# Optimization experiments

Measured on AMD Instinct MI355X. Metric: run time of the kernel, lower is better.

Reference implementation:

```python
import jax, jax.numpy as jnp
import numpy as np
from jax import lax

EPS = 1e-5      # InstanceNorm2d default eps
SLOPE = 0.2     # LeakyReLU negative slope
K = 3           # kernel size
PAD = 1


def _conv(x, w, pad=PAD):
    # x: [B,C,H,W], w: [O,I,K,K], stride 1
    return lax.conv_general_dilated(x, w, (1, 1), [(pad, pad), (pad, pad)],
                                    dimension_numbers=('NCHW', 'OIHW', 'NCHW'))


def _instance_norm(x, gamma, beta):
    mu = jnp.mean(x, (2, 3), keepdims=True)
    var = jnp.mean((x - mu) ** 2, (2, 3), keepdims=True)
    xn = (x - mu) * lax.rsqrt(var + EPS)
    return xn * gamma[None, :, None, None] + beta[None, :, None, None]


def _lrelu(x):
    return jnp.where(x >= 0, x, SLOPE * x)


def _deform_conv(x, w_off, b_off, w_def):
    # DCNv2: offsets+mask predicted by a 3x3 conv, then modulated bilinear sampling.
    B, C, H, W = x.shape
    om = _conv(x, w_off) + b_off[None, :, None, None]       # [B, 3*K*K, H, W]
    o1, o2, m = jnp.split(om, 3, axis=1)                    # each [B, K*K, H, W]
    off = jnp.concatenate([o1, o2], axis=1)                 # [B, 2*K*K, H, W]
    dy = off[:, 0::2]                                       # [B, K*K, H, W] y-offsets
    dx = off[:, 1::2]                                       # [B, K*K, H, W] x-offsets
    mask = jax.nn.sigmoid(m)                                # [B, K*K, H, W]

    ky = jnp.repeat(jnp.arange(K), K).astype(x.dtype)       # tap row index per k
    kx = jnp.tile(jnp.arange(K), K).astype(x.dtype)         # tap col index per k
    py = dy + jnp.arange(H, dtype=x.dtype)[None, None, :, None] - PAD + ky[None, :, None, None]
    px = dx + jnp.arange(W, dtype=x.dtype)[None, None, None, :] - PAD + kx[None, :, None, None]

    y0 = jnp.floor(py); x0 = jnp.floor(px)
    ly = py - y0; lx = px - x0
    y0i = y0.astype(jnp.int32); x0i = x0.astype(jnp.int32)

    xf = x.reshape(B, C, H * W)

    def gather(iy, ix):
        valid = ((iy >= 0) & (iy < H) & (ix >= 0) & (ix < W)).astype(x.dtype)
        idx = jnp.clip(iy, 0, H - 1) * W + jnp.clip(ix, 0, W - 1)
        v = jax.vmap(lambda f, i: jnp.take(f, i, axis=-1))(xf, idx)  # [B,C,K*K,H,W]
        return v * valid[:, None]

    samp = (gather(y0i, x0i)         * ((1 - ly) * (1 - lx))[:, None]
          + gather(y0i, x0i + 1)     * ((1 - ly) * lx)[:, None]
          + gather(y0i + 1, x0i)     * (ly * (1 - lx))[:, None]
          + gather(y0i + 1, x0i + 1) * (ly * lx)[:, None])          # [B,C,K*K,H,W]

    wk = w_def.reshape(w_def.shape[0], C, K * K)            # [O,C,K*K]
    return jnp.einsum('ock,bckhw,bkhw->bohw', wk, samp, mask)


def setup_inputs() -> dict:
    key = jax.random.key(0)
    ks = jax.random.split(key, 10)
    B, C, H, W = 4, 128, 96, 96
    x = jax.random.normal(ks[0], (B, C, H, W), jnp.float32)
    g1 = 1.0 + 0.05 * jax.random.normal(ks[1], (C,), jnp.float32)
    b1 = 0.05 * jax.random.normal(ks[2], (C,), jnp.float32)
    g2 = 1.0 + 0.05 * jax.random.normal(ks[3], (C,), jnp.float32)
    b2 = 0.05 * jax.random.normal(ks[4], (C,), jnp.float32)
    w1 = jax.random.normal(ks[5], (C, C, K, K), jnp.float32) * 0.03
    bc1 = 0.01 * jax.random.normal(ks[6], (C,), jnp.float32)
    # offset/mask conv: zero-init in the original; use small random values so the
    # irregular bilinear-sampling path is actually exercised.
    w_off = jax.random.normal(ks[7], (3 * K * K, C, K, K), jnp.float32) * 0.01
    b_off = 0.01 * jax.random.normal(ks[8], (3 * K * K,), jnp.float32)
    w_def = jax.random.normal(ks[9], (C, C, K, K), jnp.float32) * 0.03  # DeformConv has bias=None
    return {"x": x, "g1": g1, "b1": b1, "g2": g2, "b2": b2,
            "w1": w1, "bc1": bc1, "w_off": w_off, "b_off": b_off, "w_def": w_def}


def reference(x, g1, b1, g2, b2, w1, bc1, w_off, b_off, w_def):
    h = _lrelu(_instance_norm(x, g1, b1))
    h = _conv(h, w1) + bc1[None, :, None, None]
    h = _lrelu(_instance_norm(h, g2, b2))
    h = _deform_conv(h, w_off, b_off, w_def)
    return h + x
```

## Files before the change

kernel.cpp:

```cpp
#include <hip/hip_runtime.h>
#include <hip/hip_fp16.h>
#include <math.h>

#define HWN 9216
#define HD 96
#define WD 96

typedef _Float16 h8v __attribute__((ext_vector_type(8)));
typedef float f16x16 __attribute__((ext_vector_type(16)));

__device__ __forceinline__ ushort f2h(float f) {
  return __half_as_ushort(__float2half(f));
}
__device__ __forceinline__ __half2 u2h(unsigned u) {
  return __builtin_bit_cast(__half2, u);
}
__device__ __forceinline__ unsigned h2u(__half2 h) {
  return __builtin_bit_cast(unsigned, h);
}
__device__ __forceinline__ h8v u4h(uint4 v) {
  return __builtin_bit_cast(h8v, v);
}
__device__ __forceinline__ f16x16 mfma32(h8v a, h8v b, f16x16 c) {
  return __builtin_amdgcn_mfma_f32_32x32x16_f16(a, b, c, 0, 0, 0);
}
__device__ __forceinline__ __half2 pkmax2(__half2 a, __half2 b) {
  unsigned r;
  asm("v_pk_max_f16 %0, %1, %2" : "=v"(r) : "v"(h2u(a)), "v"(h2u(b)));
  return u2h(r);
}
__device__ __forceinline__ __half2 lrelu2(__half2 v, __half2 c02) {
  return pkmax2(v, __hmul2(v, c02));
}

__global__ __launch_bounds__(256) void packxt_kernel(
    const float* __restrict__ w1, const float* __restrict__ wdef,
    const float* __restrict__ woff, const float* __restrict__ x,
    ushort* __restrict__ w1p, ushort* __restrict__ wdp, ushort* __restrict__ wofp,
    unsigned* __restrict__ xh, float* __restrict__ partS, float* __restrict__ partQ) {
  __shared__ float tl[128][97];
  int bid = blockIdx.x;
  int t = threadIdx.x;
  if (bid < 162) {
    int i = bid * 256 + t;
    const float* src;
    ushort* dst;
    int CT, CO_real, fi;
    if (i < 18432) { src = w1; dst = w1p; CT = 4; CO_real = 128; fi = i; }
    else if (i < 36864) { src = wdef; dst = wdp; CT = 4; CO_real = 128; fi = i - 18432; }
    else { src = woff; dst = wofp; CT = 1; CO_real = 27; fi = i - 36864; }
    int lane = fi & 63;
    int j = fi >> 6;
    int ks = j & 7; j >>= 3;
    int ct = j % CT;
    int kk = j / CT;
    int co = ct * 32 + (lane & 31);
    int c0 = ks * 16 + (lane >> 5) * 8;
    ushort fr[8];
#pragma unroll
    for (int e = 0; e < 8; ++e) {
      float v = 0.f;
      if (co < CO_real) v = src[(size_t)(co * 128 + c0 + e) * 9 + kk];
      fr[e] = f2h(v);
    }
    uint4 o4;
    o4.x = (unsigned)fr[0] | ((unsigned)fr[1] << 16);
    o4.y = (unsigned)fr[2] | ((unsigned)fr[3] << 16);
    o4.z = (unsigned)fr[4] | ((unsigned)fr[5] << 16);
    o4.w = (unsigned)fr[6] | ((unsigned)fr[7] << 16);
    *(uint4*)(dst + (size_t)fi * 8) = o4;
    return;
  }
  int xb = bid - 162;
  int b = xb / 96, y = xb % 96;
  const float* sbase = x + (size_t)b * 128 * HWN + y * WD;
  for (int i = t; i < 12288; i += 256) {
    int c = i / 96, xx = i - c * 96;
    tl[c][xx] = sbase[(size_t)c * HWN + xx];
  }
  __syncthreads();
  {
    int c = t >> 1, half = t & 1;
    float S = 0.f, Q = 0.f;
    for (int j = 0; j < 48; ++j) {
      float v = tl[c][half * 48 + j];
      S += v;
      Q += v * v;
    }
    S += __shfl_xor(S, 1, 64);
    Q += __shfl_xor(Q, 1, 64);
    if (half == 0) {
      partS[((size_t)(b * 96 + y)) * 128 + c] = S;
      partQ[((size_t)(b * 96 + y)) * 128 + c] = Q;
    }
  }
  unsigned* dbase = xh + (size_t)(b * 96 + y) * 96 * 64;
  for (int i = t; i < 6144; i += 256) {
    int xx = i >> 6, c2 = i & 63;
    unsigned lo = f2h(tl[2 * c2][xx]);
    unsigned hi = f2h(tl[2 * c2 + 1][xx]);
    dbase[xx * 64 + c2] = lo | (hi << 16);
  }
}

__global__ __launch_bounds__(64) void finalize_kernel(
    const float* __restrict__ partS, const float* __restrict__ partQ,
    const float* __restrict__ gamma, const float* __restrict__ beta,
    float* __restrict__ sa_, float* __restrict__ sb_, int ntiles) {
  int bc = blockIdx.x;
  int b = bc >> 7, c = bc & 127;
  float S = 0.f, Q = 0.f;
  for (int tl = threadIdx.x; tl < ntiles; tl += 64) {
    S += partS[((size_t)b * ntiles + tl) * 128 + c];
    Q += partQ[((size_t)b * ntiles + tl) * 128 + c];
  }
#pragma unroll
  for (int off = 32; off > 0; off >>= 1) {
    S += __shfl_down(S, off, 64);
    Q += __shfl_down(Q, off, 64);
  }
  if (threadIdx.x == 0) {
    float mu = S / (float)HWN;
    float var = Q / (float)HWN - mu * mu;
    float rs = rsqrtf(var + 1e-5f);
    float a = rs * gamma[c];
    sa_[bc] = a;
    sb_[bc] = beta[c] - mu * a;
  }
}

__global__ __launch_bounds__(512) void conv1_mfma(
    const ushort* __restrict__ inp, const float* __restrict__ sa_,
    const float* __restrict__ sb_, const ushort* __restrict__ wp,
    const float* __restrict__ bias, ushort* __restrict__ outh,
    float* __restrict__ partS, float* __restrict__ partQ) {
  __shared__ ushort halo[100 * 128];
  __shared__ __half2 sah[64], sbh[64];
  int b = blockIdx.y;
  int tile = blockIdx.x;
  int Y0 = (tile / 12) * 8, X0 = (tile % 12) * 8;
  int t = threadIdx.x;
  int lane = t & 63, w = t >> 6;
  if (t < 64) {
    sah[t] = __floats2half2_rn(sa_[b * 128 + 2 * t], sa_[b * 128 + 2 * t + 1]);
    sbh[t] = __floats2half2_rn(sb_[b * 128 + 2 * t], sb_[b * 128 + 2 * t + 1]);
  }
  __syncthreads();
  const __half2 c02 = __float2half2_rn(0.2f);
  const ushort* ib = inp + (size_t)b * HWN * 128;
  for (int i = t; i < 400; i += 512) {
    int r = i >> 2, q = i & 3;
    int gy = Y0 - 1 + r / 10, gx = X0 - 1 + r % 10;
    bool inb = ((unsigned)gy < 96u) && ((unsigned)gx < 96u);
    const uint4* gp4 = (const uint4*)(ib + (size_t)(gy * 96 + gx) * 128 + q * 32);
#pragma unroll
    for (int cc = 0; cc < 4; ++cc) {
      uint4 v = make_uint4(0, 0, 0, 0);
      if (inb) {
        uint4 g = gp4[cc];
        unsigned ar[4] = {g.x, g.y, g.z, g.w};
        int c2b = (q * 4 + cc) * 4;
#pragma unroll
        for (int j = 0; j < 4; ++j) {
          __half2 hv = __hfma2(u2h(ar[j]), sah[c2b + j], sbh[c2b + j]);
          hv = lrelu2(hv, c02);
          ar[j] = h2u(hv);
        }
        v.x = ar[0]; v.y = ar[1]; v.z = ar[2]; v.w = ar[3];
      }
      int ch = (q * 4 + cc) ^ (r & 7);
      *(uint4*)&halo[r * 128 + ch * 8] = v;
    }
  }
  __syncthreads();

  int ct = w >> 1, pt = w & 1;
  int pl = lane & 31, kh = lane >> 5;
  int p = pt * 32 + pl;
  f16x16 acc = (f16x16)(0.f);

  uint4 Acur[8], Anxt[8];
#pragma unroll
  for (int ks = 0; ks < 8; ++ks)
    Acur[ks] = *(const uint4*)(wp + (size_t)((0 * 4 + ct) * 8 + ks) * 512 + lane * 8);

  for (int kk = 0; kk < 9; ++kk) {
    if (kk < 8) {
#pragma unroll
      for (int ks = 0; ks < 8; ++ks)
        Anxt[ks] = *(const uint4*)(wp + (size_t)(((kk + 1) * 4 + ct) * 8 + ks) * 512 + lane * 8);
    }
    int ky = kk / 3, kx = kk % 3;
    int r = ((p >> 3) + ky) * 10 + (p & 7) + kx;
    __builtin_amdgcn_s_setprio(1);
#pragma unroll
    for (int ks = 0; ks < 8; ++ks) {
      int u = (ks * 2 + kh) ^ (r & 7);
      h8v bf = *(const h8v*)&halo[r * 128 + u * 8];
      acc = mfma32(u4h(Acur[ks]), bf, acc);
    }
    __builtin_amdgcn_s_setprio(0);
    if (kk < 8) {
#pragma unroll
      for (int ks = 0; ks < 8; ++ks) Acur[ks] = Anxt[ks];
    }
  }
  int gp = (Y0 + (p >> 3)) * 96 + X0 + (p & 7);
  float s[16], q[16];
#pragma unroll
  for (int g = 0; g < 4; ++g) {
    int ch0 = ct * 32 + 4 * kh + 8 * g;
    float v0 = acc[4 * g + 0] + bias[ch0 + 0];
    float v1 = acc[4 * g + 1] + bias[ch0 + 1];
    float v2 = acc[4 * g + 2] + bias[ch0 + 2];
    float v3 = acc[4 * g + 3] + bias[ch0 + 3];
    uint2 o;
    o.x = (unsigned)f2h(v0) | ((unsigned)f2h(v1) << 16);
    o.y = (unsigned)f2h(v2) | ((unsigned)f2h(v3) << 16);
    *(uint2*)&outh[((size_t)b * HWN + gp) * 128 + ch0] = o;
    s[4 * g + 0] = v0; s[4 * g + 1] = v1; s[4 * g + 2] = v2; s[4 * g + 3] = v3;
    q[4 * g + 0] = v0 * v0; q[4 * g + 1] = v1 * v1;
    q[4 * g + 2] = v2 * v2; q[4 * g + 3] = v3 * v3;
  }
#pragma unroll
  for (int r = 0; r < 16; ++r)
#pragma unroll
    for (int m = 1; m < 32; m <<= 1) {
      s[r] += __shfl_xor(s[r], m, 64);
      q[r] += __shfl_xor(q[r], m, 64);
    }
  if (pl == 0) {
    size_t base = ((size_t)b * 288 + tile * 2 + pt) * 128;
#pragma unroll
    for (int r = 0; r < 16; ++r) {
      int co = ct * 32 + 4 * kh + (r & 3) + 8 * (r >> 2);
      partS[base + co] = s[r];
      partQ[base + co] = q[r];
    }
  }
}

__device__ __forceinline__ uint4 gaffine(const ushort* hb, int pix, int cc,
                                         const __half2* sa2v, const __half2* sb2v,
                                         __half2 c02) {
  uint4 g = *(const uint4*)(hb + (size_t)pix * 128 + cc * 8);
  unsigned ar[4] = {g.x, g.y, g.z, g.w};
#pragma unroll
  for (int j = 0; j < 4; ++j) {
    __half2 hv = __hfma2(u2h(ar[j]), sa2v[j], sb2v[j]);
    hv = lrelu2(hv, c02);
    ar[j] = h2u(hv);
  }
  return make_uint4(ar[0], ar[1], ar[2], ar[3]);
}

__global__ __launch_bounds__(256) void deform_fused(
    const ushort* __restrict__ h2n, const float* __restrict__ sa_,
    const float* __restrict__ sb_, const ushort* __restrict__ wofp,
    const float* __restrict__ boff, const ushort* __restrict__ wdp,
    const float* __restrict__ x, float* __restrict__ out) {
  __shared__ __align__(16) ushort halo[96 * 128];
  __shared__ __align__(16) ushort S[32 * 128];
  __shared__ __align__(16) ushort4 idxs[9][32];
  __shared__ __align__(16) ushort4 wgtc[9][32];
  __shared__ __half2 sah[64], sbh[64];
  float* om_t = (float*)S;
  int bid = blockIdx.x;
  int swz = (bid & 7) * 144 + (bid >> 3);
  int b = swz / 288;
  int tile = swz % 288;
  int Y0 = (tile / 12) * 4, X0 = (tile % 12) * 8;
  int t = threadIdx.x;
  int lane = t & 63, w = t >> 6;
  const ushort* hb = h2n + (size_t)b * HWN * 128;
  if (t < 64) {
    sah[t] = __floats2half2_rn(sa_[b * 128 + 2 * t], sa_[b * 128 + 2 * t + 1]);
    sbh[t] = __floats2half2_rn(sb_[b * 128 + 2 * t], sb_[b * 128 + 2 * t + 1]);
  }
  __syncthreads();
  const __half2 c02 = __float2half2_rn(0.2f);

  for (int i = t; i < 1536; i += 256) {
    int pix = i >> 4, u = i & 15;
    int gy = Y0 - 2 + pix / 12, gx = X0 - 2 + pix % 12;
    uint4 v = make_uint4(0, 0, 0, 0);
    if (((unsigned)gy < 96u) && ((unsigned)gx < 96u)) {
      uint4 g = *(const uint4*)(hb + (size_t)(gy * 96 + gx) * 128 + u * 8);
      unsigned ar[4] = {g.x, g.y, g.z, g.w};
#pragma unroll
      for (int j = 0; j < 4; ++j) {
        __half2 hv = __hfma2(u2h(ar[j]), sah[u * 4 + j], sbh[u * 4 + j]);
        hv = lrelu2(hv, c02);
        ar[j] = h2u(hv);
      }
      v.x = ar[0]; v.y = ar[1]; v.z = ar[2]; v.w = ar[3];
    }
    *(uint4*)&halo[pix * 128 + ((u ^ (pix & 15)) * 8)] = v;
  }
  __syncthreads();

  if (w == 0) {
    int pl = lane & 31, kh = lane >> 5;
    int p = pl;
    f16x16 accm = (f16x16)(0.f);
    uint4 Ac[8], An[8];
#pragma unroll
    for (int ks = 0; ks < 8; ++ks)
      Ac[ks] = *(const uint4*)(wofp + (size_t)(0 * 8 + ks) * 512 + lane * 8);
    for (int kk = 0; kk < 9; ++kk) {
      if (kk < 8) {
#pragma unroll
        for (int ks = 0; ks < 8; ++ks)
          An[ks] = *(const uint4*)(wofp + (size_t)((kk + 1) * 8 + ks) * 512 + lane * 8);
      }
      int ky = kk / 3, kx = kk % 3;
      int hp = (1 + (p >> 3) + ky) * 12 + 1 + (p & 7) + kx;
#pragma unroll
      for (int ks = 0; ks < 8; ++ks) {
        int u = (ks * 2 + kh) ^ (hp & 15);
        h8v bf = *(const h8v*)&halo[hp * 128 + u * 8];
        accm = mfma32(u4h(Ac[ks]), bf, accm);
      }
      if (kk < 8) {
#pragma unroll
        for (int ks = 0; ks < 8; ++ks) Ac[ks] = An[ks];
      }
    }
#pragma unroll
    for (int reg = 0; reg < 16; ++reg) {
      int co = 4 * kh + (reg & 3) + 8 * (reg >> 2);
      if (co < 27) om_t[co * 32 + p] = accm[reg] + boff[co];
    }
  }
  __syncthreads();

  for (int i = t; i < 288; i += 256) {
    int k = i >> 5, p = i & 31;
    int yy = Y0 + (p >> 3), xx = X0 + (p & 7);
    float dy = om_t[(2 * k) * 32 + p];
    float dx = om_t[(2 * k + 1) * 32 + p];
    float mv = om_t[(18 + k) * 32 + p];
    float mask = 1.0f / (1.0f + expf(-mv));
    float py = dy + (float)(yy - 1 + (k / 3));
    float px = dx + (float)(xx - 1 + (k % 3));
    float fy = floorf(py), fx = floorf(px);
    float lyf = py - fy, lxf = px - fx;
    int y0 = (int)fy, x0 = (int)fx;
    int y1 = y0 + 1, x1 = x0 + 1;
    bool vy0 = (y0 >= 0) && (y0 < HD);
    bool vy1 = (y1 >= 0) && (y1 < HD);
    bool vx0 = (x0 >= 0) && (x0 < WD);
    bool vx1 = (x1 >= 0) && (x1 < WD);
    int y0c = min(max(y0, 0), HD - 1), y1c = min(max(y1, 0), HD - 1);
    int x0c = min(max(x0, 0), WD - 1), x1c = min(max(x1, 0), WD - 1);
    float w0 = (1.f - lyf) * (1.f - lxf) * ((vy0 && vx0) ? mask : 0.f);
    float w1v = (1.f - lyf) * lxf * ((vy0 && vx1) ? mask : 0.f);
    float w2 = lyf * (1.f - lxf) * ((vy1 && vx0) ? mask : 0.f);
    float w3 = lyf * lxf * ((vy1 && vx1) ? mask : 0.f);
    bool inh = (y0c >= Y0 - 2) && (y1c <= Y0 + 5) && (x0c >= X0 - 2) && (x1c <= X0 + 9);
    ushort4 sidx;
    if (inh) {
      int sy0 = y0c - (Y0 - 2), sy1 = y1c - (Y0 - 2);
      int sx0 = x0c - (X0 - 2), sx1 = x1c - (X0 - 2);
      sidx.x = (ushort)(sy0 * 12 + sx0);
      sidx.y = (ushort)(sy0 * 12 + sx1);
      sidx.z = (ushort)(sy1 * 12 + sx0);
      sidx.w = (ushort)(sy1 * 12 + sx1);
    } else {
      sidx.x = (ushort)((y0c * WD + x0c) | 0x8000);
      sidx.y = (ushort)(y0c * WD + x1c);
      sidx.z = (ushort)(y1c * WD + x0c);
      sidx.w = (ushort)(y1c * WD + x1c);
    }
    idxs[k][p] = sidx;
    ushort4 wc;
    wc.x = f2h(w0); wc.y = f2h(w1v); wc.z = f2h(w2); wc.w = f2h(w3);
    wgtc[k][p] = wc;
  }
  __syncthreads();

  int cc = t & 15;
  int pp = t >> 4;
  int ct = w;
  int pl = lane & 31, kh = lane >> 5;
  int pg = pl;
  f16x16 acc = (f16x16)(0.f);
  __half2 sa2v[4], sb2v[4];
#pragma unroll
  for (int j = 0; j < 4; ++j) { sa2v[j] = sah[cc * 4 + j]; sb2v[j] = sbh[cc * 4 + j]; }

  uint4 AW[8];
  for (int k = 0; k < 9; ++k) {
    const ushort* wk = wdp + (size_t)k * 16384;
#pragma unroll
    for (int ks = 0; ks < 8; ++ks)
      AW[ks] = *(const uint4*)(wk + (size_t)(ct * 8 + ks) * 512 + lane * 8);
#pragma unroll
    for (int i2 = 0; i2 < 2; ++i2) {
      int p = pp + 16 * i2;
      ushort4 sidx = idxs[k][p];
      ushort4 wc = wgtc[k][p];
      uint4 C0, C1, C2, C3;
      if (sidx.x & 0x8000u) {
        C0 = gaffine(hb, sidx.x & 0x7fff, cc, sa2v, sb2v, c02);
        C1 = gaffine(hb, sidx.y, cc, sa2v, sb2v, c02);
        C2 = gaffine(hb, sidx.z, cc, sa2v, sb2v, c02);
        C3 = gaffine(hb, sidx.w, cc, sa2v, sb2v, c02);
      } else {
        C0 = *(const uint4*)&halo[sidx.x * 128 + ((cc ^ (sidx.x & 15)) * 8)];
        C1 = *(const uint4*)&halo[sidx.y * 128 + ((cc ^ (sidx.y & 15)) * 8)];
        C2 = *(const uint4*)&halo[sidx.z * 128 + ((cc ^ (sidx.z & 15)) * 8)];
        C3 = *(const uint4*)&halo[sidx.w * 128 + ((cc ^ (sidx.w & 15)) * 8)];
      }
      __half2 a0 = u2h((unsigned)wc.x * 0x10001u);
      __half2 a1 = u2h((unsigned)wc.y * 0x10001u);
      __half2 a2 = u2h((unsigned)wc.z * 0x10001u);
      __half2 a3 = u2h((unsigned)wc.w * 0x10001u);
      __half2 s0 = __hmul2(u2h(C0.x), a0);
      __half2 s1 = __hmul2(u2h(C0.y), a0);
      __half2 s2 = __hmul2(u2h(C0.z), a0);
      __half2 s3 = __hmul2(u2h(C0.w), a0);
      s0 = __hfma2(u2h(C1.x), a1, s0); s1 = __hfma2(u2h(C1.y), a1, s1);
      s2 = __hfma2(u2h(C1.z), a1, s2); s3 = __hfma2(u2h(C1.w), a1, s3);
      s0 = __hfma2(u2h(C2.x), a2, s0); s1 = __hfma2(u2h(C2.y), a2, s1);
      s2 = __hfma2(u2h(C2.z), a2, s2); s3 = __hfma2(u2h(C2.w), a2, s3);
      s0 = __hfma2(u2h(C3.x), a3, s0); s1 = __hfma2(u2h(C3.y), a3, s1);
      s2 = __hfma2(u2h(C3.z), a3, s2); s3 = __hfma2(u2h(C3.w), a3, s3);
      uint4 o4;
      o4.x = h2u(s0); o4.y = h2u(s1); o4.z = h2u(s2); o4.w = h2u(s3);
      *(uint4*)&S[p * 128 + ((cc ^ (p & 15)) * 8)] = o4;
    }
    asm volatile("s_waitcnt lgkmcnt(0)" ::: "memory");
    __builtin_amdgcn_s_barrier();
#pragma unroll
    for (int ks = 0; ks < 8; ++ks) {
      int u = (ks * 2 + kh) ^ (pg & 15);
      h8v bf = *(const h8v*)&S[pg * 128 + u * 8];
      acc = mfma32(u4h(AW[ks]), bf, acc);
    }
    asm volatile("s_waitcnt lgkmcnt(0)" ::: "memory");
    __builtin_amdgcn_s_barrier();
  }
  int gp = (Y0 + (pg >> 3)) * 96 + X0 + (pg & 7);
#pragma unroll
  for (int reg = 0; reg < 16; ++reg) {
    int co = ct * 32 + 4 * kh + (reg & 3) + 8 * (reg >> 2);
    size_t oi = (size_t)(b * 128 + co) * HWN + gp;
    out[oi] = acc[reg] + x[oi];
  }
}

extern "C" void kernel_launch(void* const* d_in, const int* in_sizes, int n_in,
                              void* d_out, int out_size, void* d_ws, size_t ws_size,
                              hipStream_t stream) {
  const float* x = (const float*)d_in[0];
  const float* g1 = (const float*)d_in[1];
  const float* b1 = (const float*)d_in[2];
  const float* g2 = (const float*)d_in[3];
  const float* b2 = (const float*)d_in[4];
  const float* w1 = (const float*)d_in[5];
  const float* bc1 = (const float*)d_in[6];
  const float* w_off = (const float*)d_in[7];
  const float* b_off = (const float*)d_in[8];
  const float* w_def = (const float*)d_in[9];
  float* out = (float*)d_out;
  float* ws = (float*)d_ws;

  ushort* w1p = (ushort*)ws;
  ushort* wofp = (ushort*)(ws + 73728);
  ushort* wdp = (ushort*)(ws + 92160);
  float* sa1 = ws + 165888;
  float* sb1 = ws + 166400;
  float* sa2 = ws + 166912;
  float* sb2 = ws + 167424;
  float* partS1 = ws + 167936;
  float* partQ1 = ws + 217088;
  float* partS2 = ws + 266240;
  float* partQ2 = ws + 413696;
  ushort* xh = (ushort*)(ws + 561152);
  ushort* hBh = (ushort*)(ws + 2920448);

  packxt_kernel<<<546, 256, 0, stream>>>(w1, w_def, w_off, x, w1p, wdp, wofp,
                                         (unsigned*)xh, partS1, partQ1);
  finalize_kernel<<<512, 64, 0, stream>>>(partS1, partQ1, g1, b1, sa1, sb1, 96);
  conv1_mfma<<<dim3(144, 4), 512, 0, stream>>>(xh, sa1, sb1, w1p, bc1, hBh, partS2, partQ2);
  finalize_kernel<<<512, 64, 0, stream>>>(partS2, partQ2, g2, b2, sa2, sb2, 288);
  deform_fused<<<dim3(1152), 256, 0, stream>>>(hBh, sa2, sb2, wofp, b_off, wdp, x, out);
}
```

Baseline: 89.58 us.

## Move instance-norm stats out of conv1 into a separate stats kernel

The per-tile sum and sum-of-squares reduction in conv1's epilogue, with its many cross-lane shuffles, is replaced by a standalone stats2_kernel that re-reads the fp16 conv1 output and writes 64 partials per image instead of 288. The deform kernel also prefetches the residual x values before its main loop and raises wave priority around the MFMA section. This trades an extra kernel launch and a full re-read of hBh against a lighter conv1 epilogue. Statistics are now computed from fp16-rounded values rather than fp32 accumulators, which slightly changes the numerics.

Result: faster. 83.12 us (-7.2%).

```diff
diff --git a/kernel.cpp b/kernel.cpp
--- a/kernel.cpp
+++ b/kernel.cpp
@@ -129,11 +129,55 @@
   }
 }
 
+__global__ __launch_bounds__(256) void stats2_kernel(
+    const ushort* __restrict__ hBh, float* __restrict__ partS,
+    float* __restrict__ partQ) {
+  int tile = blockIdx.x;
+  int b = blockIdx.y;
+  int t = threadIdx.x;
+  int cc = t & 15, pp = t >> 4;
+  int wid = t >> 6, lane = t & 63;
+  const ushort* base = hBh + ((size_t)b * HWN + tile * 144) * 128 + cc * 8;
+  float S[8], Q[8];
+#pragma unroll
+  for (int e = 0; e < 8; ++e) { S[e] = 0.f; Q[e] = 0.f; }
+  for (int i = 0; i < 9; ++i) {
+    int pix = i * 16 + pp;
+    uint4 v = *(const uint4*)(base + (size_t)pix * 128);
+    unsigned ar[4] = {v.x, v.y, v.z, v.w};
+#pragma unroll
+    for (int j = 0; j < 4; ++j) {
+      float2 f = __half22float2(u2h(ar[j]));
+      S[2 * j] += f.x; Q[2 * j] += f.x * f.x;
+      S[2 * j + 1] += f.y; Q[2 * j + 1] += f.y * f.y;
+    }
+  }
+#pragma unroll
+  for (int e = 0; e < 8; ++e) {
+    S[e] += __shfl_xor(S[e], 16, 64); Q[e] += __shfl_xor(Q[e], 16, 64);
+    S[e] += __shfl_xor(S[e], 32, 64); Q[e] += __shfl_xor(Q[e], 32, 64);
+  }
+  __shared__ float red[2][4][16][8];
+  if (lane < 16) {
+#pragma unroll
+    for (int e = 0; e < 8; ++e) { red[0][wid][lane][e] = S[e]; red[1][wid][lane][e] = Q[e]; }
+  }
+  __syncthreads();
+  if (t < 16) {
+#pragma unroll
+    for (int e = 0; e < 8; ++e) {
+      float s = red[0][0][t][e] + red[0][1][t][e] + red[0][2][t][e] + red[0][3][t][e];
+      float q = red[1][0][t][e] + red[1][1][t][e] + red[1][2][t][e] + red[1][3][t][e];
+      partS[((size_t)b * 64 + tile) * 128 + t * 8 + e] = s;
+      partQ[((size_t)b * 64 + tile) * 128 + t * 8 + e] = q;
+    }
+  }
+}
+
 __global__ __launch_bounds__(512) void conv1_mfma(
     const ushort* __restrict__ inp, const float* __restrict__ sa_,
     const float* __restrict__ sb_, const ushort* __restrict__ wp,
-    const float* __restrict__ bias, ushort* __restrict__ outh,
-    float* __restrict__ partS, float* __restrict__ partQ) {
+    const float* __restrict__ bias, ushort* __restrict__ outh) {
   __shared__ ushort halo[100 * 128];
   __shared__ __half2 sah[64], sbh[64];
   int b = blockIdx.y;
@@ -206,7 +250,6 @@
     }
   }
   int gp = (Y0 + (p >> 3)) * 96 + X0 + (p & 7);
-  float s[16], q[16];
 #pragma unroll
   for (int g = 0; g < 4; ++g) {
     int ch0 = ct * 32 + 4 * kh + 8 * g;
@@ -218,25 +261,6 @@
     o.x = (unsigned)f2h(v0) | ((unsigned)f2h(v1) << 16);
     o.y = (unsigned)f2h(v2) | ((unsigned)f2h(v3) << 16);
     *(uint2*)&outh[((size_t)b * HWN + gp) * 128 + ch0] = o;
-    s[4 * g + 0] = v0; s[4 * g + 1] = v1; s[4 * g + 2] = v2; s[4 * g + 3] = v3;
-    q[4 * g + 0] = v0 * v0; q[4 * g + 1] = v1 * v1;
-    q[4 * g + 2] = v2 * v2; q[4 * g + 3] = v3 * v3;
-  }
-#pragma unroll
-  for (int r = 0; r < 16; ++r)
-#pragma unroll
-    for (int m = 1; m < 32; m <<= 1) {
-      s[r] += __shfl_xor(s[r], m, 64);
-      q[r] += __shfl_xor(q[r], m, 64);
-    }
-  if (pl == 0) {
-    size_t base = ((size_t)b * 288 + tile * 2 + pt) * 128;
-#pragma unroll
-    for (int r = 0; r < 16; ++r) {
-      int co = ct * 32 + 4 * kh + (r & 3) + 8 * (r >> 2);
-      partS[base + co] = s[r];
-      partQ[base + co] = q[r];
-    }
   }
 }
 
@@ -389,6 +413,14 @@
 #pragma unroll
   for (int j = 0; j < 4; ++j) { sa2v[j] = sah[cc * 4 + j]; sb2v[j] = sbh[cc * 4 + j]; }
 
+  int gp = (Y0 + (pg >> 3)) * 96 + X0 + (pg & 7);
+  float xr[16];
+#pragma unroll
+  for (int reg = 0; reg < 16; ++reg) {
+    int co = ct * 32 + 4 * kh + (reg & 3) + 8 * (reg >> 2);
+    xr[reg] = x[(size_t)(b * 128 + co) * HWN + gp];
+  }
+
   uint4 AW[8];
   for (int k = 0; k < 9; ++k) {
     const ushort* wk = wdp + (size_t)k * 16384;
@@ -432,21 +464,22 @@
     }
     asm volatile("s_waitcnt lgkmcnt(0)" ::: "memory");
     __builtin_amdgcn_s_barrier();
+    __builtin_amdgcn_s_setprio(1);
 #pragma unroll
     for (int ks = 0; ks < 8; ++ks) {
       int u = (ks * 2 + kh) ^ (pg & 15);
       h8v bf = *(const h8v*)&S[pg * 128 + u * 8];
       acc = mfma32(u4h(AW[ks]), bf, acc);
     }
+    __builtin_amdgcn_s_setprio(0);
     asm volatile("s_waitcnt lgkmcnt(0)" ::: "memory");
     __builtin_amdgcn_s_barrier();
   }
-  int gp = (Y0 + (pg >> 3)) * 96 + X0 + (pg & 7);
 #pragma unroll
   for (int reg = 0; reg < 16; ++reg) {
     int co = ct * 32 + 4 * kh + (reg & 3) + 8 * (reg >> 2);
     size_t oi = (size_t)(b * 128 + co) * HWN + gp;
-    out[oi] = acc[reg] + x[oi];
+    out[oi] = acc[reg] + xr[reg];
   }
 }
 
@@ -476,14 +509,15 @@
   float* partS1 = ws + 167936;
   float* partQ1 = ws + 217088;
   float* partS2 = ws + 266240;
-  float* partQ2 = ws + 413696;
-  ushort* xh = (ushort*)(ws + 561152);
-  ushort* hBh = (ushort*)(ws + 2920448);
+  float* partQ2 = ws + 299008;
+  ushort* xh = (ushort*)(ws + 331776);
+  ushort* hBh = (ushort*)(ws + 2691072);
 
   packxt_kernel<<<546, 256, 0, stream>>>(w1, w_def, w_off, x, w1p, wdp, wofp,
                                          (unsigned*)xh, partS1, partQ1);
   finalize_kernel<<<512, 64, 0, stream>>>(partS1, partQ1, g1, b1, sa1, sb1, 96);
-  conv1_mfma<<<dim3(144, 4), 512, 0, stream>>>(xh, sa1, sb1, w1p, bc1, hBh, partS2, partQ2);
-  finalize_kernel<<<512, 64, 0, stream>>>(partS2, partQ2, g2, b2, sa2, sb2, 288);
+  conv1_mfma<<<dim3(144, 4), 512, 0, stream>>>(xh, sa1, sb1, w1p, bc1, hBh);
+  stats2_kernel<<<dim3(64, 4), 256, 0, stream>>>(hBh, partS2, partQ2);
+  finalize_kernel<<<512, 64, 0, stream>>>(partS2, partQ2, g2, b2, sa2, sb2, 64);
   deform_fused<<<dim3(1152), 256, 0, stream>>>(hBh, sa2, sb2, wofp, b_off, wdp, x, out);
 }
```
